# Optimization experiments

Measured on AMD Instinct MI355X. Metric: run time of the kernel, lower is better.

The kernel has to match this reference:

```python
import jax, jax.numpy as jnp
import numpy as np

B, T, C = 32, 256, 512
MAX_LEN = 25


def setup_inputs() -> dict:
    key = jax.random.key(0)
    ks = jax.random.split(key, 6)
    scale = 1.0 / np.sqrt(C)
    return {
        "word_features": jax.random.normal(ks[0], (B, T, C), dtype=jnp.float32),
        "word_fc_w": jax.random.normal(ks[1], (C, C), dtype=jnp.float32) * scale,
        "word_fc_b": jax.random.normal(ks[2], (C,), dtype=jnp.float32) * scale,
        "pos_emb": jax.random.normal(ks[3], (MAX_LEN, C), dtype=jnp.float32),
        "atten_w": jax.random.normal(ks[4], (C,), dtype=jnp.float32) * scale,
        "atten_b": jax.random.normal(ks[5], (1,), dtype=jnp.float32) * scale,
    }


def reference(word_features, word_fc_w, word_fc_b, pos_emb, atten_w, atten_b):
    # word_fc: (b,t,c) -> (b,t,c)
    wf = jnp.einsum("btc,dc->btd", word_features, word_fc_w) + word_fc_b
    # additive (Bahdanau) attention scores over t for each of max_len query positions
    # add_features: (b, L, t, c) = wf[:,None,:,:] + pos_emb[None,:,None,:]
    add_features = jnp.tanh(wf[:, None, :, :] + pos_emb[None, :, None, :])
    # atten_fc: (b, L, t, 1) -> squeeze -> (b, L, t)
    scores = jnp.einsum("bltc,c->blt", add_features, atten_w) + atten_b[0]
    attn = jax.nn.softmax(scores, axis=2)  # softmax over t
    # bmm: (b,L,t) @ (b,t,c) -> (b,L,c)
    pvam_features = jnp.einsum("blt,btc->blc", attn, wf)
    return pvam_features
```

## Files before the change

### kernel.cpp

```cpp
#include <hip/hip_runtime.h>

#define Bn 32
#define Tn 256
#define Cn 512
#define Ln 25
#define K2n 1024

typedef __attribute__((ext_vector_type(8))) short sh8;
typedef __attribute__((ext_vector_type(4))) float f32x4;

#define SCALE2LOG2E 2.885390081777927f

#if __has_builtin(__builtin_amdgcn_exp2f)
#define EXP2(x) __builtin_amdgcn_exp2f(x)
#else
#define EXP2(x) __expf(0.69314718056f * (x))
#endif

#define DPP_ADD(v, ctrl) \
    ((v) + __int_as_float(__builtin_amdgcn_update_dpp(0, __float_as_int(v), ctrl, 0xf, 0xf, true)))

__device__ __forceinline__ unsigned short f2bf(float f) {
    unsigned u = __float_as_uint(f);
    u += 0x7FFF + ((u >> 16) & 1);
    return (unsigned short)(u >> 16);
}
__device__ __forceinline__ float bf2f(unsigned short b) {
    return __uint_as_float(((unsigned)b) << 16);
}

#define NA_QUAD (Bn * Tn * Cn / 4)
#define NW_QUAD (Cn * Cn / 4)
__global__ __launch_bounds__(256) void k_convert(
        const float* __restrict__ A, const float* __restrict__ W,
        unsigned short* __restrict__ A2, unsigned short* __restrict__ W2) {
    int idx = blockIdx.x * 256 + threadIdx.x;
    if (idx < NA_QUAD) {
        int m = idx >> 7, kq = (idx & 127) << 2;
        float4 a = *(const float4*)&A[m * Cn + kq];
        sh8 o;
        float v[4] = {a.x, a.y, a.z, a.w};
        #pragma unroll
        for (int i = 0; i < 4; ++i) {
            unsigned short hi = f2bf(v[i]);
            unsigned short lo = f2bf(v[i] - bf2f(hi));
            o[2 * i] = (short)hi; o[2 * i + 1] = (short)lo;
        }
        *(sh8*)&A2[(size_t)m * K2n + kq * 2] = o;
    } else {
        int j = idx - NA_QUAD;
        int n = j >> 7, kq = (j & 127) << 2;
        float4 w = *(const float4*)&W[n * Cn + kq];
        sh8 o;
        float v[4] = {w.x, w.y, w.z, w.w};
        #pragma unroll
        for (int i = 0; i < 4; ++i) {
            short b = (short)f2bf(v[i]);
            o[2 * i] = b; o[2 * i + 1] = b;
        }
        *(sh8*)&W2[(size_t)n * K2n + kq * 2] = o;
    }
}

#define BM 128
#define BN 64
#define BKg 64
__global__ __launch_bounds__(256) void k_gemm(
        const unsigned short* __restrict__ A2, const unsigned short* __restrict__ W2,
        const float* __restrict__ bias, float* __restrict__ wf) {
    __shared__ unsigned short As[BM * BKg];
    __shared__ unsigned short Ws[BN * BKg];
    const int tid  = threadIdx.x;
    const int lane = tid & 63;
    const int wv   = tid >> 6;
    const int m0 = blockIdx.y * BM;
    const int n0 = blockIdx.x * BN;
    const int wm = (wv >> 1) * 64;
    const int wn = (wv & 1) * 32;
    const int r = lane & 15, q = lane >> 4;

    const unsigned short* gA[4];
    const unsigned short* gW[2];
    #pragma unroll
    for (int rr = 0; rr < 4; ++rr) {
        int p = rr * 256 + tid;
        int row = p >> 3, pk = p & 7;
        int lk = pk ^ (row & 7);
        gA[rr] = A2 + (size_t)(m0 + row) * K2n + lk * 8;
    }
    #pragma unroll
    for (int rr = 0; rr < 2; ++rr) {
        int p = rr * 256 + tid;
        int row = p >> 3, pk = p & 7;
        int lk = pk ^ (row & 7);
        gW[rr] = W2 + (size_t)(n0 + row) * K2n + lk * 8;
    }

    f32x4 acc[4][2];
    #pragma unroll
    for (int mi = 0; mi < 4; ++mi)
        #pragma unroll
        for (int ni = 0; ni < 2; ++ni) acc[mi][ni] = (f32x4){0.f, 0.f, 0.f, 0.f};

    for (int kt = 0; kt < K2n / BKg; ++kt) {
        __syncthreads();
        #pragma unroll
        for (int rr = 0; rr < 4; ++rr) {
            __builtin_amdgcn_global_load_lds(
                (const __attribute__((address_space(1))) unsigned int*)gA[rr],
                (__attribute__((address_space(3))) unsigned int*)(As + (rr * 256 + wv * 64) * 8),
                16, 0, 0);
            gA[rr] += BKg;
        }
        #pragma unroll
        for (int rr = 0; rr < 2; ++rr) {
            __builtin_amdgcn_global_load_lds(
                (const __attribute__((address_space(1))) unsigned int*)gW[rr],
                (__attribute__((address_space(3))) unsigned int*)(Ws + (rr * 256 + wv * 64) * 8),
                16, 0, 0);
            gW[rr] += BKg;
        }
        __syncthreads();

        sh8 af[4][2], bfr[2][2];
        #pragma unroll
        for (int mi = 0; mi < 4; ++mi)
            #pragma unroll
            for (int kk = 0; kk < 2; ++kk) {
                int row = wm + mi * 16 + r;
                int phys = (kk * 4 + q) ^ (r & 7);
                af[mi][kk] = *(const sh8*)&As[row * BKg + phys * 8];
            }
        #pragma unroll
        for (int ni = 0; ni < 2; ++ni)
            #pragma unroll
            for (int kk = 0; kk < 2; ++kk) {
                int row = wn + ni * 16 + r;
                int phys = (kk * 4 + q) ^ (r & 7);
                bfr[ni][kk] = *(const sh8*)&Ws[row * BKg + phys * 8];
            }
        #pragma unroll
        for (int kk = 0; kk < 2; ++kk)
            #pragma unroll
            for (int mi = 0; mi < 4; ++mi)
                #pragma unroll
                for (int ni = 0; ni < 2; ++ni)
                    acc[mi][ni] = __builtin_amdgcn_mfma_f32_16x16x32_bf16(
                        af[mi][kk], bfr[ni][kk], acc[mi][ni], 0, 0, 0);
    }

    #pragma unroll
    for (int ni = 0; ni < 2; ++ni) {
        const float bv = bias[n0 + wn + ni * 16 + r];
        #pragma unroll
        for (int mi = 0; mi < 4; ++mi)
            #pragma unroll
            for (int reg = 0; reg < 4; ++reg) {
                int row = m0 + wm + mi * 16 + q * 4 + reg;
                int col = n0 + wn + ni * 16 + r;
                wf[(size_t)row * Cn + col] = acc[mi][ni][reg] + bv;
            }
    }
}

__global__ __launch_bounds__(512) void k_scores(
        const float* __restrict__ wf, const float* __restrict__ pos,
        const float* __restrict__ aw, float* __restrict__ scores4) {
    __shared__ float pos2[Ln * Cn];
    const int tid = threadIdx.x;
    for (int i = tid * 4; i < Ln * Cn; i += 2048) {
        float4 p = *(const float4*)&pos[i];
        p.x *= SCALE2LOG2E; p.y *= SCALE2LOG2E; p.z *= SCALE2LOG2E; p.w *= SCALE2LOG2E;
        *(float4*)&pos2[i] = p;
    }
    __syncthreads();

    const int lane = tid & 63;
    const int wv   = tid >> 6;
    const int t    = blockIdx.x * 8 + wv;
    const int b    = blockIdx.y;

    const float* wfp = wf + (b * Tn + t) * Cn;
    float4 w0 = *(const float4*)&wfp[lane * 4];
    float4 w1 = *(const float4*)&wfp[256 + lane * 4];
    w0.x *= SCALE2LOG2E; w0.y *= SCALE2LOG2E; w0.z *= SCALE2LOG2E; w0.w *= SCALE2LOG2E;
    w1.x *= SCALE2LOG2E; w1.y *= SCALE2LOG2E; w1.z *= SCALE2LOG2E; w1.w *= SCALE2LOG2E;
    const float4 a0 = *(const float4*)&aw[lane * 4];
    const float4 a1 = *(const float4*)&aw[256 + lane * 4];
    const float U = a0.x + a0.y + a0.z + a0.w + a1.x + a1.y + a1.z + a1.w;
    float4 u0, u1;
    u0.x = -2.f * a0.x; u0.y = -2.f * a0.y; u0.z = -2.f * a0.z; u0.w = -2.f * a0.w;
    u1.x = -2.f * a1.x; u1.y = -2.f * a1.y; u1.z = -2.f * a1.z; u1.w = -2.f * a1.w;

    float* sp = scores4 + ((lane >> 4) * (Bn * Ln * Tn)) + (b * Ln) * Tn + t;
    const bool writer = ((lane & 15) == 0);

    #pragma unroll
    for (int l = 0; l < Ln; ++l) {
        const float4 p0 = *(const float4*)&pos2[l * Cn + lane * 4];
        const float4 p1 = *(const float4*)&pos2[l * Cn + 256 + lane * 4];
        float s = U;
        s = fmaf(u0.x, __builtin_amdgcn_rcpf(1.f + EXP2(w0.x + p0.x)), s);
        s = fmaf(u0.y, __builtin_amdgcn_rcpf(1.f + EXP2(w0.y + p0.y)), s);
        s = fmaf(u0.z, __builtin_amdgcn_rcpf(1.f + EXP2(w0.z + p0.z)), s);
        s = fmaf(u0.w, __builtin_amdgcn_rcpf(1.f + EXP2(w0.w + p0.w)), s);
        s = fmaf(u1.x, __builtin_amdgcn_rcpf(1.f + EXP2(w1.x + p1.x)), s);
        s = fmaf(u1.y, __builtin_amdgcn_rcpf(1.f + EXP2(w1.y + p1.y)), s);
        s = fmaf(u1.z, __builtin_amdgcn_rcpf(1.f + EXP2(w1.z + p1.z)), s);
        s = fmaf(u1.w, __builtin_amdgcn_rcpf(1.f + EXP2(w1.w + p1.w)), s);
        s = DPP_ADD(s, 0xB1);
        s = DPP_ADD(s, 0x4E);
        s = DPP_ADD(s, 0x141);
        s = DPP_ADD(s, 0x140);
        if (writer) sp[l * Tn] = s;
    }
}

__global__ __launch_bounds__(512) void k_pvam(
        const float* __restrict__ wf, const float* __restrict__ scores4,
        float* __restrict__ out) {
    __shared__ float buf[8 * Ln * 64];
    __shared__ float pT[Tn][28];
    const int tid = threadIdx.x;
    const int cx  = blockIdx.x;
    const int b   = blockIdx.y;

    const float* sc = scores4 + b * Ln * Tn;
    const int PL = Bn * Ln * Tn;
    for (int i = tid * 4; i < Ln * Tn; i += 2048) {
        float4 s0 = *(const float4*)&sc[i];
        float4 s1 = *(const float4*)&sc[PL + i];
        float4 s2 = *(const float4*)&sc[2 * PL + i];
        float4 s3 = *(const float4*)&sc[3 * PL + i];
        float4 v;
        v.x = (s0.x + s1.x) + (s2.x + s3.x);
        v.y = (s0.y + s1.y) + (s2.y + s3.y);
        v.z = (s0.z + s1.z) + (s2.z + s3.z);
        v.w = (s0.w + s1.w) + (s2.w + s3.w);
        *(float4*)&buf[i] = v;
    }
    __syncthreads();

    const int lane = tid & 63;
    const int wv   = tid >> 6;

    for (int l = wv; l < Ln; l += 8) {
        float v0 = buf[l * Tn + lane];
        float v1 = buf[l * Tn + 64 + lane];
        float v2 = buf[l * Tn + 128 + lane];
        float v3 = buf[l * Tn + 192 + lane];
        float m = fmaxf(fmaxf(v0, v1), fmaxf(v2, v3));
        #pragma unroll
        for (int o = 32; o > 0; o >>= 1) m = fmaxf(m, __shfl_xor(m, o));
        float e0 = __expf(v0 - m), e1 = __expf(v1 - m);
        float e2 = __expf(v2 - m), e3 = __expf(v3 - m);
        float s = e0 + e1 + e2 + e3;
        #pragma unroll
        for (int o = 32; o > 0; o >>= 1) s += __shfl_xor(s, o);
        float rs = __builtin_amdgcn_rcpf(s);
        pT[lane][l]       = e0 * rs;
        pT[64 + lane][l]  = e1 * rs;
        pT[128 + lane][l] = e2 * rs;
        pT[192 + lane][l] = e3 * rs;
    }
    __syncthreads();

    const int c = cx * 64 + lane;
    float acc[Ln];
    #pragma unroll
    for (int l = 0; l < Ln; ++l) acc[l] = 0.f;

    const float* wfp = wf + (b * Tn + wv * 32) * Cn + c;
    for (int tt = 0; tt < 32; ++tt) {
        float w = wfp[tt * Cn];
        const float* pp = &pT[wv * 32 + tt][0];
        float p[Ln];
        *(float4*)&p[0]  = *(const float4*)&pp[0];
        *(float4*)&p[4]  = *(const float4*)&pp[4];
        *(float4*)&p[8]  = *(const float4*)&pp[8];
        *(float4*)&p[12] = *(const float4*)&pp[12];
        *(float4*)&p[16] = *(const float4*)&pp[16];
        *(float4*)&p[20] = *(const float4*)&pp[20];
        p[24] = pp[24];
        #pragma unroll
        for (int l = 0; l < Ln; ++l) acc[l] = fmaf(p[l], w, acc[l]);
    }

    __syncthreads();
    #pragma unroll
    for (int l = 0; l < Ln; ++l)
        buf[(wv * Ln + l) * 64 + lane] = acc[l];
    __syncthreads();
    for (int idx = tid; idx < Ln * 64; idx += 512) {
        int l = idx >> 6, cc = idx & 63;
        float v = 0.f;
        #pragma unroll
        for (int w = 0; w < 8; ++w) v += buf[(w * Ln + l) * 64 + cc];
        out[(b * Ln + l) * Cn + cx * 64 + cc] = v;
    }
}

extern "C" void kernel_launch(void* const* d_in, const int* in_sizes, int n_in,
                              void* d_out, int out_size, void* d_ws, size_t ws_size,
                              hipStream_t stream) {
    const float* A    = (const float*)d_in[0];
    const float* W    = (const float*)d_in[1];
    const float* bias = (const float*)d_in[2];
    const float* pos  = (const float*)d_in[3];
    const float* aw   = (const float*)d_in[4];

    char* ws = (char*)d_ws;
    float*          wf      = (float*)ws;
    float*          scores4 = (float*)(ws + 16777216ull);
    unsigned short* A2      = (unsigned short*)(ws + 20054016ull);
    unsigned short* W2      = (unsigned short*)(ws + 36831232ull);
    float* out = (float*)d_out;

    k_convert<<<(NA_QUAD + NW_QUAD) / 256, 256, 0, stream>>>(A, W, A2, W2);
    k_gemm<<<dim3(Cn / BN, (Bn * Tn) / BM), 256, 0, stream>>>(A2, W2, bias, wf);
    k_scores<<<dim3(Tn / 8, Bn), 512, 0, stream>>>(wf, pos, aw, scores4);
    k_pvam<<<dim3(Cn / 64, Bn), 512, 0, stream>>>(wf, scores4, out);
}
```

Before: 136.0 us.

## Split scores over channel halves, stream pos from global, reduce partials in LDS

k_scores no longer stages the whole 25x512 position table in shared memory per block. Each wave now handles half the channels of one t and streams pos rows from global memory with a one-row prefetch. The per-wave partial sums are reduced in shared memory and written as a single scores array, so k_pvam no longer has to sum four partial planes. This cuts per-block LDS fill cost and shrinks the scores workspace, at the price of twice as many blocks, repeated global pos reads served from cache, and an added barrier.

```diff
diff --git a/kernel.cpp b/kernel.cpp
--- a/kernel.cpp
+++ b/kernel.cpp
@@ -165,59 +165,54 @@
 
 __global__ __launch_bounds__(512) void k_scores(
         const float* __restrict__ wf, const float* __restrict__ pos,
-        const float* __restrict__ aw, float* __restrict__ scores4) {
-    __shared__ float pos2[Ln * Cn];
-    const int tid = threadIdx.x;
-    for (int i = tid * 4; i < Ln * Cn; i += 2048) {
-        float4 p = *(const float4*)&pos[i];
-        p.x *= SCALE2LOG2E; p.y *= SCALE2LOG2E; p.z *= SCALE2LOG2E; p.w *= SCALE2LOG2E;
-        *(float4*)&pos2[i] = p;
-    }
-    __syncthreads();
-
+        const float* __restrict__ aw, float* __restrict__ scores) {
+    __shared__ float part[4 * Ln * 8];
+    const int tid  = threadIdx.x;
     const int lane = tid & 63;
     const int wv   = tid >> 6;
-    const int t    = blockIdx.x * 8 + wv;
+    const int tl   = wv >> 1;
+    const int ch   = wv & 1;
+    const int t    = blockIdx.x * 4 + tl;
     const int b    = blockIdx.y;
-
-    const float* wfp = wf + (b * Tn + t) * Cn;
-    float4 w0 = *(const float4*)&wfp[lane * 4];
-    float4 w1 = *(const float4*)&wfp[256 + lane * 4];
-    w0.x *= SCALE2LOG2E; w0.y *= SCALE2LOG2E; w0.z *= SCALE2LOG2E; w0.w *= SCALE2LOG2E;
-    w1.x *= SCALE2LOG2E; w1.y *= SCALE2LOG2E; w1.z *= SCALE2LOG2E; w1.w *= SCALE2LOG2E;
-    const float4 a0 = *(const float4*)&aw[lane * 4];
-    const float4 a1 = *(const float4*)&aw[256 + lane * 4];
-    const float U = a0.x + a0.y + a0.z + a0.w + a1.x + a1.y + a1.z + a1.w;
-    float4 u0, u1;
-    u0.x = -2.f * a0.x; u0.y = -2.f * a0.y; u0.z = -2.f * a0.z; u0.w = -2.f * a0.w;
-    u1.x = -2.f * a1.x; u1.y = -2.f * a1.y; u1.z = -2.f * a1.z; u1.w = -2.f * a1.w;
-
-    float* sp = scores4 + ((lane >> 4) * (Bn * Ln * Tn)) + (b * Ln) * Tn + t;
-    const bool writer = ((lane & 15) == 0);
-
-    #pragma unroll
+    const int co   = ch * 256 + lane * 4;
+
+    float4 w = *(const float4*)&wf[(b * Tn + t) * Cn + co];
+    w.x *= SCALE2LOG2E; w.y *= SCALE2LOG2E; w.z *= SCALE2LOG2E; w.w *= SCALE2LOG2E;
+    const float4 a = *(const float4*)&aw[co];
+    const float U = (a.x + a.y) + (a.z + a.w);
+    float4 u;
+    u.x = -2.f * a.x; u.y = -2.f * a.y; u.z = -2.f * a.z; u.w = -2.f * a.w;
+
+    const float* pp = pos + co;
+    float4 p = *(const float4*)pp;
+    #pragma unroll 1
     for (int l = 0; l < Ln; ++l) {
-        const float4 p0 = *(const float4*)&pos2[l * Cn + lane * 4];
-        const float4 p1 = *(const float4*)&pos2[l * Cn + 256 + lane * 4];
+        float4 pn = p;
+        if (l < Ln - 1) pn = *(const float4*)(pp + (l + 1) * Cn);
         float s = U;
-        s = fmaf(u0.x, __builtin_amdgcn_rcpf(1.f + EXP2(w0.x + p0.x)), s);
-        s = fmaf(u0.y, __builtin_amdgcn_rcpf(1.f + EXP2(w0.y + p0.y)), s);
-        s = fmaf(u0.z, __builtin_amdgcn_rcpf(1.f + EXP2(w0.z + p0.z)), s);
-        s = fmaf(u0.w, __builtin_amdgcn_rcpf(1.f + EXP2(w0.w + p0.w)), s);
-        s = fmaf(u1.x, __builtin_amdgcn_rcpf(1.f + EXP2(w1.x + p1.x)), s);
-        s = fmaf(u1.y, __builtin_amdgcn_rcpf(1.f + EXP2(w1.y + p1.y)), s);
-        s = fmaf(u1.z, __builtin_amdgcn_rcpf(1.f + EXP2(w1.z + p1.z)), s);
-        s = fmaf(u1.w, __builtin_amdgcn_rcpf(1.f + EXP2(w1.w + p1.w)), s);
+        s = fmaf(u.x, __builtin_amdgcn_rcpf(1.f + EXP2(fmaf(SCALE2LOG2E, p.x, w.x))), s);
+        s = fmaf(u.y, __builtin_amdgcn_rcpf(1.f + EXP2(fmaf(SCALE2LOG2E, p.y, w.y))), s);
+        s = fmaf(u.z, __builtin_amdgcn_rcpf(1.f + EXP2(fmaf(SCALE2LOG2E, p.z, w.z))), s);
+        s = fmaf(u.w, __builtin_amdgcn_rcpf(1.f + EXP2(fmaf(SCALE2LOG2E, p.w, w.w))), s);
         s = DPP_ADD(s, 0xB1);
         s = DPP_ADD(s, 0x4E);
         s = DPP_ADD(s, 0x141);
         s = DPP_ADD(s, 0x140);
-        if (writer) sp[l * Tn] = s;
+        if ((lane & 15) == 0)
+            part[(tl * Ln + l) * 8 + ch * 4 + (lane >> 4)] = s;
+        p = pn;
+    }
+    __syncthreads();
+    if (tid < 4 * Ln) {
+        int tl2 = tid / Ln, l2 = tid - tl2 * Ln;
+        const float* q = &part[(tl2 * Ln + l2) * 8];
+        float v = ((q[0] + q[1]) + (q[2] + q[3])) + ((q[4] + q[5]) + (q[6] + q[7]));
+        scores[(b * Ln + l2) * Tn + blockIdx.x * 4 + tl2] = v;
     }
 }
 
 __global__ __launch_bounds__(512) void k_pvam(
-        const float* __restrict__ wf, const float* __restrict__ scores4,
+        const float* __restrict__ wf, const float* __restrict__ scores,
         float* __restrict__ out) {
     __shared__ float buf[8 * Ln * 64];
     __shared__ float pT[Tn][28];
@@ -225,20 +220,9 @@
     const int cx  = blockIdx.x;
     const int b   = blockIdx.y;
 
-    const float* sc = scores4 + b * Ln * Tn;
-    const int PL = Bn * Ln * Tn;
-    for (int i = tid * 4; i < Ln * Tn; i += 2048) {
-        float4 s0 = *(const float4*)&sc[i];
-        float4 s1 = *(const float4*)&sc[PL + i];
-        float4 s2 = *(const float4*)&sc[2 * PL + i];
-        float4 s3 = *(const float4*)&sc[3 * PL + i];
-        float4 v;
-        v.x = (s0.x + s1.x) + (s2.x + s3.x);
-        v.y = (s0.y + s1.y) + (s2.y + s3.y);
-        v.z = (s0.z + s1.z) + (s2.z + s3.z);
-        v.w = (s0.w + s1.w) + (s2.w + s3.w);
-        *(float4*)&buf[i] = v;
-    }
+    const float* sc = scores + b * Ln * Tn;
+    for (int i = tid * 4; i < Ln * Tn; i += 2048)
+        *(float4*)&buf[i] = *(const float4*)&sc[i];
     __syncthreads();
 
     const int lane = tid & 63;
@@ -310,14 +294,14 @@
     const float* aw   = (const float*)d_in[4];
 
     char* ws = (char*)d_ws;
-    float*          wf      = (float*)ws;
-    float*          scores4 = (float*)(ws + 16777216ull);
-    unsigned short* A2      = (unsigned short*)(ws + 20054016ull);
-    unsigned short* W2      = (unsigned short*)(ws + 36831232ull);
+    float*          wf     = (float*)ws;
+    float*          scores = (float*)(ws + 16777216ull);
+    unsigned short* A2     = (unsigned short*)(ws + 20054016ull);
+    unsigned short* W2     = (unsigned short*)(ws + 36831232ull);
     float* out = (float*)d_out;
 
     k_convert<<<(NA_QUAD + NW_QUAD) / 256, 256, 0, stream>>>(A, W, A2, W2);
     k_gemm<<<dim3(Cn / BN, (Bn * Tn) / BM), 256, 0, stream>>>(A2, W2, bias, wf);
-    k_scores<<<dim3(Tn / 8, Bn), 512, 0, stream>>>(wf, pos, aw, scores4);
-    k_pvam<<<dim3(Cn / 64, Bn), 512, 0, stream>>>(wf, scores4, out);
-}
+    k_scores<<<dim3(Tn / 4, Bn), 512, 0, stream>>>(wf, pos, aw, scores);
+    k_pvam<<<dim3(Cn / 64, Bn), 512, 0, stream>>>(wf, scores, out);
+}
```

New measurement: 136.2 us. Within noise of the previous version (+0.2%).
